# Performance work log

Hardware: AMD Instinct MI355X
Metric: run time of the kernel (lower is better)

Reference implementation:

```python
import jax, jax.numpy as jnp
import numpy as np

NUM_HEADS = 16
D_MODEL = 1024
DEPTH = D_MODEL // NUM_HEADS


def rope_sincos(seq_len, depth):
    # standard RoPE: inv_freq over even dims, sin/cos tiled to full depth
    inv_freq = 1.0 / (10000.0 ** (jnp.arange(0, depth, 2, dtype=jnp.float32) / depth))
    ang = jnp.arange(seq_len, dtype=jnp.float32)[:, None] * inv_freq[None, :]  # [S, depth/2]
    sin = jnp.concatenate([jnp.sin(ang), jnp.sin(ang)], axis=-1)  # [S, depth]
    cos = jnp.concatenate([jnp.cos(ang), jnp.cos(ang)], axis=-1)
    return sin, cos


def apply_rope(x, sin, cos):
    # x: [B,H,S,depth]; rotate-half formulation
    half = x.shape[-1] // 2
    x1, x2 = x[..., :half], x[..., half:]
    rot = jnp.concatenate([-x2, x1], axis=-1)
    return x * cos + rot * sin


def setup_inputs() -> dict:
    key = jax.random.key(0)
    ks = jax.random.split(key, 5)
    s = 1.0 / np.sqrt(D_MODEL)
    return {
        "x": jax.random.normal(ks[0], (2, 2048, D_MODEL), dtype=jnp.float32),
        "wq": jax.random.normal(ks[1], (D_MODEL, D_MODEL), dtype=jnp.float32) * s,
        "bq": jnp.zeros((D_MODEL,), jnp.float32),
        "wk": jax.random.normal(ks[2], (D_MODEL, D_MODEL), dtype=jnp.float32) * s,
        "bk": jnp.zeros((D_MODEL,), jnp.float32),
        "wv": jax.random.normal(ks[3], (D_MODEL, D_MODEL), dtype=jnp.float32) * s,
        "bv": jnp.zeros((D_MODEL,), jnp.float32),
        "wo": jax.random.normal(ks[4], (D_MODEL, D_MODEL), dtype=jnp.float32) * s,
        "bo": jnp.zeros((D_MODEL,), jnp.float32),
    }


def reference(x, wq, bq, wk, bk, wv, bv, wo, bo):
    B, S, _ = x.shape

    def split_heads(t):  # [B,S,D] -> [B,H,S,depth]
        return t.reshape(B, S, NUM_HEADS, DEPTH).transpose(0, 2, 1, 3)

    Q = split_heads(x @ wq + bq)
    K = split_heads(x @ wk + bk)
    V = split_heads(x @ wv + bv)

    sin, cos = rope_sincos(S, DEPTH)  # [S, depth], broadcasts over B,H
    Q = apply_rope(Q, sin, cos)
    K = apply_rope(K, sin, cos)

    scores = jnp.einsum("bhqd,bhkd->bhqk", Q, K) / jnp.sqrt(jnp.float32(DEPTH))
    weights = jax.nn.softmax(scores, axis=-1)
    out = jnp.einsum("bhqk,bhkd->bhqd", weights, V)
    out = out.transpose(0, 2, 1, 3).reshape(B, S, D_MODEL)
    return out @ wo + bo
```

## Files before the change

### kernel.cpp

```cpp
#include <hip/hip_runtime.h>

#define DM 1024
#define SEQ 2048
#define NH 16
#define DH 64
#define BATCH 2

typedef _Float16 half_t;
typedef _Float16 half8 __attribute__((ext_vector_type(8)));
typedef _Float16 half4 __attribute__((ext_vector_type(4)));
typedef __fp16 f16x2 __attribute__((ext_vector_type(2)));
typedef unsigned u32x2 __attribute__((ext_vector_type(2)));
typedef unsigned u32x4 __attribute__((ext_vector_type(4)));
typedef float f32x4 __attribute__((ext_vector_type(4)));

__device__ __forceinline__ f32x4 mfma16(half8 a, half8 b, f32x4 c) {
  return __builtin_amdgcn_mfma_f32_16x16x32_f16(a, b, c, 0, 0, 0);
}
__device__ __forceinline__ f32x4 mfma16k16(half4 a, half4 b, f32x4 c) {
  return __builtin_amdgcn_mfma_f32_16x16x16f16(a, b, c, 0, 0, 0);
}

__device__ __forceinline__ void gl2lds16(const half_t* g, half_t* l) {
  __builtin_amdgcn_global_load_lds((const __attribute__((address_space(1))) void*)g,
                                   (__attribute__((address_space(3))) void*)l, 16, 0, 0);
}


__global__ __launch_bounds__(256)
void prep_kernel(const float* __restrict__ x,
                 const float* __restrict__ w0, const float* __restrict__ w1,
                 const float* __restrict__ w2, const float* __restrict__ w3,
                 half_t* __restrict__ xh,
                 half_t* __restrict__ o0, half_t* __restrict__ o1,
                 half_t* __restrict__ o2, half_t* __restrict__ o3,
                 float* __restrict__ st, float* __restrict__ ct) {
  __shared__ float tile[32][33];
  const int lid = blockIdx.x;
  const int tid = threadIdx.x;
  if (lid < 4096) {
    int i = (lid * 256 + tid) * 4;
    float4 v = *(const float4*)(x + i);
    half4 h = { (half_t)v.x, (half_t)v.y, (half_t)v.z, (half_t)v.w };
    *(half4*)(xh + i) = h;
  } else if (lid < 8192) {
    int l = lid - 4096;
    int z = l >> 10;
    int by = (l >> 5) & 31, bx = l & 31;
    const float* w = (z == 0) ? w0 : (z == 1) ? w1 : (z == 2) ? w2 : w3;
    half_t* o = (z == 0) ? o0 : (z == 1) ? o1 : (z == 2) ? o2 : o3;
    int tx = tid & 31, ty0 = tid >> 5;
    int bxx = bx * 32, byy = by * 32;
#pragma unroll
    for (int i = 0; i < 4; i++) {
      int ty = ty0 + i * 8;
      tile[ty][tx] = w[(size_t)(byy + ty) * DM + bxx + tx];
    }
    __syncthreads();
#pragma unroll
    for (int i = 0; i < 4; i++) {
      int ty = ty0 + i * 8;
      o[(size_t)(bxx + ty) * DM + byy + tx] = (half_t)tile[tx][ty];
    }
  } else {
    int idx = (lid - 8192) * 256 + tid;
    int s = idx >> 5, i = idx & 31;
    float freq = exp2f(-(float)i * (13.287712379549449f / 32.0f));
    float ang = (float)s * freq;
    st[idx] = sinf(ang);
    ct[idx] = cosf(ang);
  }
}


__global__ __launch_bounds__(256)
void qkv_kernel(const half_t* __restrict__ xh,
                const half_t* __restrict__ wtq, const half_t* __restrict__ wtk,
                const half_t* __restrict__ wtv,
                const float* __restrict__ bq, const float* __restrict__ bk,
                const float* __restrict__ bv,
                const float* __restrict__ st, const float* __restrict__ ctab,
                half_t* __restrict__ Qh, half_t* __restrict__ Kh, half_t* __restrict__ Vt) {
  const int tid = threadIdx.x;
  const int wid = tid >> 6, lane = tid & 63;
  const int l16 = lane & 15, quad = lane >> 4;
  const int m0 = blockIdx.y * 128, n0 = blockIdx.x * 128;
  const int g = blockIdx.z;
  const half_t* wt = (g == 0) ? wtq : (g == 1) ? wtk : wtv;
  const float* bias = (g == 0) ? bq : (g == 1) ? bk : bv;
  __shared__ __align__(16) char smem[32768];
  f32x4 acc[4][4] = {};
  const int wrow = (wid >> 1) * 64, wcol = (wid & 1) * 64;

  const int ar0 = tid >> 2,          ab0 = (tid & 3) ^ ((ar0 >> 1) & 3);
  const int ar1 = (tid + 256) >> 2,  ab1 = (tid & 3) ^ ((ar1 >> 1) & 3);
  const int swz = (l16 >> 1) & 3;

  {
    half_t* As = (half_t*)smem;
    half_t* Bs = (half_t*)(smem + 16384);
    gl2lds16(&xh[(size_t)(m0 + ar0) * DM + ab0 * 8], &As[tid * 8]);
    gl2lds16(&xh[(size_t)(m0 + ar1) * DM + ab1 * 8], &As[(tid + 256) * 8]);
    gl2lds16(&wt[(size_t)(n0 + ar0) * DM + ab0 * 8], &Bs[tid * 8]);
    gl2lds16(&wt[(size_t)(n0 + ar1) * DM + ab1 * 8], &Bs[(tid + 256) * 8]);
  }
  __syncthreads();

  int cur = 0;
  for (int k0 = 0; k0 < DM; k0 += 32) {
    if (k0 + 32 < DM) {
      half_t* Asn = (half_t*)(smem + (cur ^ 1) * 8192);
      half_t* Bsn = (half_t*)(smem + 16384 + (cur ^ 1) * 8192);
      const int kn = k0 + 32;
      gl2lds16(&xh[(size_t)(m0 + ar0) * DM + kn + ab0 * 8], &Asn[tid * 8]);
      gl2lds16(&xh[(size_t)(m0 + ar1) * DM + kn + ab1 * 8], &Asn[(tid + 256) * 8]);
      gl2lds16(&wt[(size_t)(n0 + ar0) * DM + kn + ab0 * 8], &Bsn[tid * 8]);
      gl2lds16(&wt[(size_t)(n0 + ar1) * DM + kn + ab1 * 8], &Bsn[(tid + 256) * 8]);
    }
    const half_t* Asc = (const half_t*)(smem + cur * 8192);
    const half_t* Bsc = (const half_t*)(smem + 16384 + cur * 8192);
    half8 a[4], b[4];
#pragma unroll
    for (int rt = 0; rt < 4; rt++)
      a[rt] = *(const half8*)&Asc[((wrow + rt * 16 + l16) * 4 + (quad ^ swz)) * 8];
#pragma unroll
    for (int ct = 0; ct < 4; ct++)
      b[ct] = *(const half8*)&Bsc[((wcol + ct * 16 + l16) * 4 + (quad ^ swz)) * 8];
#pragma unroll
    for (int rt = 0; rt < 4; rt++)
#pragma unroll
      for (int ct = 0; ct < 4; ct++)
        acc[rt][ct] = mfma16(a[rt], b[ct], acc[rt][ct]);
    __syncthreads();
    cur ^= 1;
  }

  const int h = (n0 + wcol) >> 6;
  const float qscale = 0.125f * 1.44269504089f;
  float bv4[4];
#pragma unroll
  for (int ct = 0; ct < 4; ct++) bv4[ct] = bias[n0 + wcol + ct * 16 + l16];

  if (g == 2) {
    half_t* vt = (half_t*)(smem + wid * 8192);
#pragma unroll
    for (int rt = 0; rt < 4; rt++)
#pragma unroll
      for (int ct = 0; ct < 4; ct++) {
        half4 hv;
#pragma unroll
        for (int r = 0; r < 4; r++) hv[r] = (half_t)(acc[rt][ct][r] + bv4[ct]);
        int row = ct * 16 + l16;
        int colu = rt * 2 + (quad >> 1);
        *(half4*)&vt[row * 64 + ((colu ^ (row & 7)) * 8) + (quad & 1) * 4] = hv;
      }
    const int sb = m0 + wrow;
    const int bb = sb >> 11, s0 = sb & 2047;
    half_t* dstv = Vt + (size_t)(bb * NH + h) * DH * SEQ;
#pragma unroll
    for (int i = 0; i < 8; i++) {
      int d = i * 8 + (lane >> 3), c = lane & 7;
      half8 v = *(const half8*)&vt[d * 64 + ((c ^ (d & 7)) * 8)];
      *(half8*)&dstv[(size_t)d * SEQ + s0 + c * 8] = v;
    }
  } else {
    half_t* dst = (g == 0) ? Qh : Kh;
#pragma unroll
    for (int rt = 0; rt < 4; rt++) {
#pragma unroll
      for (int r = 0; r < 4; r++) {
        int m = m0 + wrow + rt * 16 + quad * 4 + r;
        int bb = m >> 11, s = m & 2047;
        float v0 = acc[rt][0][r] + bv4[0];
        float v1 = acc[rt][1][r] + bv4[1];
        float v2 = acc[rt][2][r] + bv4[2];
        float v3 = acc[rt][3][r] + bv4[3];
        float sn0 = st[s * 32 + l16], cs0 = ctab[s * 32 + l16];
        float sn1 = st[s * 32 + 16 + l16], cs1 = ctab[s * 32 + 16 + l16];
        float o0 = v0 * cs0 - v2 * sn0;
        float o1 = v1 * cs1 - v3 * sn1;
        float o2 = v2 * cs0 + v0 * sn0;
        float o3 = v3 * cs1 + v1 * sn1;
        if (g == 0) { o0 *= qscale; o1 *= qscale; o2 *= qscale; o3 *= qscale; }
        size_t base = ((size_t)(bb * NH + h) * SEQ + s) * DH;
        dst[base + l16]      = (half_t)o0;
        dst[base + 16 + l16] = (half_t)o1;
        dst[base + 32 + l16] = (half_t)o2;
        dst[base + 48 + l16] = (half_t)o3;
      }
    }
  }
}


__global__ __launch_bounds__(256)
void attn_kernel(const half_t* __restrict__ Qh, const half_t* __restrict__ Kh,
                 const half_t* __restrict__ Vt, half_t* __restrict__ AO) {
  const int tid = threadIdx.x;
  const int wid = tid >> 6, lane = tid & 63;
  const int l16 = lane & 15, quad = lane >> 4;
  const int lid = blockIdx.x;
  const int bh = lid & 31, qt = lid >> 5;
  const int bb = bh >> 4, h = bh & 15;
  const int q0 = qt * 128 + wid * 32;
  const half_t* Q = Qh + (size_t)bh * SEQ * DH;
  const half_t* K = Kh + (size_t)bh * SEQ * DH;
  const half_t* V = Vt + (size_t)bh * DH * SEQ;
  __shared__ __align__(16) half_t Ks[2][64 * 64];
  __shared__ __align__(16) half_t Vs[2][64 * 64];

  const int r0 = tid >> 3,         c0 = (tid & 7) ^ (r0 & 7);
  const int r1 = (tid + 256) >> 3, c1 = (tid & 7) ^ (r1 & 7);
  const int sw0 = ((quad ^ (l16 & 7)) * 8);
  const int sw1 = (((quad + 4) ^ (l16 & 7)) * 8);

  const half_t* gK0 = &K[(size_t)r0 * DH + c0 * 8];
  const half_t* gK1 = &K[(size_t)r1 * DH + c1 * 8];
  const half_t* gV0 = &V[(size_t)r0 * SEQ + c0 * 8];
  const half_t* gV1 = &V[(size_t)r1 * SEQ + c1 * 8];

  half8 aqA[2], aqB[2];
#pragma unroll
  for (int rt = 0; rt < 2; rt++) {
    aqA[rt] = *(const half8*)&Q[(size_t)(q0 + rt * 16 + l16) * DH + quad * 8];
    aqB[rt] = *(const half8*)&Q[(size_t)(q0 + rt * 16 + l16) * DH + 32 + quad * 8];
  }

  f32x4 o[2][4] = {};
  f32x4 vsum[2] = {};
  const f32x4 cinit = {-12.f, -12.f, -12.f, -12.f};

  gl2lds16(gK0, &Ks[0][tid * 8]);
  gl2lds16(gK1, &Ks[0][(tid + 256) * 8]);
  gl2lds16(gV0, &Vs[0][tid * 8]);
  gl2lds16(gV1, &Vs[0][(tid + 256) * 8]);
  __syncthreads();

  int cur = 0;
  for (int kb0 = 0; kb0 < SEQ; kb0 += 64) {
    const bool pf = (kb0 + 64 < SEQ);
    u32x4 rk0, rk1, rv0, rv1;
    if (pf) {
      const int kb = kb0 + 64;
      rk0 = *(const u32x4*)(gK0 + (size_t)kb * DH);
      rk1 = *(const u32x4*)(gK1 + (size_t)kb * DH);
      rv0 = *(const u32x4*)(gV0 + kb);
      rv1 = *(const u32x4*)(gV1 + kb);
    }
    const half_t* ksrc = Ks[cur];
    const half_t* vsrc = Vs[cur];

    f32x4 z[2][4];
    __builtin_amdgcn_s_setprio(1);
#pragma unroll
    for (int kt = 0; kt < 4; kt++) {
      const half_t* krow = &ksrc[(kt * 16 + l16) * 64];
      half8 b0 = *(const half8*)&krow[sw0];
      half8 b1 = *(const half8*)&krow[sw1];
#pragma unroll
      for (int rt = 0; rt < 2; rt++) {
        f32x4 zz = cinit;
        zz = mfma16(b0, aqA[rt], zz);
        zz = mfma16(b1, aqB[rt], zz);
        z[rt][kt] = zz;
      }
    }
    __builtin_amdgcn_s_setprio(0);

    half4 pa[2][4];
#pragma unroll
    for (int rt = 0; rt < 2; rt++)
#pragma unroll
      for (int kt = 0; kt < 4; kt++) {
        f32x4 p;
#pragma unroll
        for (int r = 0; r < 4; r++) p[r] = __builtin_amdgcn_exp2f(z[rt][kt][r]);
        vsum[rt] += p;
        f16x2 lo = __builtin_amdgcn_cvt_pkrtz(p[0], p[1]);
        f16x2 hi = __builtin_amdgcn_cvt_pkrtz(p[2], p[3]);
        u32x2 w = { __builtin_bit_cast(unsigned, lo), __builtin_bit_cast(unsigned, hi) };
        pa[rt][kt] = __builtin_bit_cast(half4, w);
      }

    __builtin_amdgcn_s_setprio(1);
#pragma unroll
    for (int dt = 0; dt < 4; dt++) {
      const int row = dt * 16 + l16;
      const half_t* vrow = &vsrc[row * 64 + (quad & 1) * 4];
#pragma unroll
      for (int kt = 0; kt < 4; kt++) {
        half4 bv = *(const half4*)&vrow[((kt * 2 + (quad >> 1)) ^ (l16 & 7)) * 8];
#pragma unroll
        for (int rt = 0; rt < 2; rt++)
          o[rt][dt] = mfma16k16(pa[rt][kt], bv, o[rt][dt]);
      }
    }
    __builtin_amdgcn_s_setprio(0);

    if (pf) {
      const int nxt = cur ^ 1;
      *(u32x4*)&Ks[nxt][tid * 8] = rk0;
      *(u32x4*)&Ks[nxt][(tid + 256) * 8] = rk1;
      *(u32x4*)&Vs[nxt][tid * 8] = rv0;
      *(u32x4*)&Vs[nxt][(tid + 256) * 8] = rv1;
    }
    __syncthreads();
    cur ^= 1;
  }

  float linv[2][4];
#pragma unroll
  for (int rt = 0; rt < 2; rt++) {
    float s = (vsum[rt][0] + vsum[rt][1]) + (vsum[rt][2] + vsum[rt][3]);
    s += __shfl_xor(s, 16);
    s += __shfl_xor(s, 32);
#pragma unroll
    for (int r = 0; r < 4; r++) linv[rt][r] = 1.f / __shfl(s, quad * 4 + r);
  }
#pragma unroll
  for (int rt = 0; rt < 2; rt++)
#pragma unroll
    for (int dt = 0; dt < 4; dt++)
#pragma unroll
      for (int r = 0; r < 4; r++) {
        int srow = q0 + rt * 16 + quad * 4 + r;
        AO[((size_t)bb * SEQ + srow) * DM + h * DH + dt * 16 + l16] =
            (half_t)(o[rt][dt][r] * linv[rt][r]);
      }
}


__global__ __launch_bounds__(256)
void out_kernel(const half_t* __restrict__ AO, const half_t* __restrict__ wto,
                const float* __restrict__ bo, float* __restrict__ out) {
  const int tid = threadIdx.x;
  const int wid = tid >> 6, lane = tid & 63;
  const int l16 = lane & 15, quad = lane >> 4;
  const int m0 = blockIdx.y * 128, n0 = blockIdx.x * 64;
  __shared__ __align__(16) char smem[24576];
  f32x4 acc[4][2] = {};
  const int wrow = (wid >> 1) * 64, wcol = (wid & 1) * 32;

  const int ar0 = tid >> 2,         ab0 = (tid & 3) ^ ((ar0 >> 1) & 3);
  const int ar1 = (tid + 256) >> 2, ab1 = (tid & 3) ^ ((ar1 >> 1) & 3);
  const int swz = (l16 >> 1) & 3;

  {
    half_t* As = (half_t*)smem;
    half_t* Bs = (half_t*)(smem + 16384);
    gl2lds16(&AO[(size_t)(m0 + ar0) * DM + ab0 * 8], &As[tid * 8]);
    gl2lds16(&AO[(size_t)(m0 + ar1) * DM + ab1 * 8], &As[(tid + 256) * 8]);
    gl2lds16(&wto[(size_t)(n0 + ar0) * DM + ab0 * 8], &Bs[tid * 8]);
  }
  __syncthreads();

  int cur = 0;
  for (int k0 = 0; k0 < DM; k0 += 32) {
    if (k0 + 32 < DM) {
      half_t* Asn = (half_t*)(smem + (cur ^ 1) * 8192);
      half_t* Bsn = (half_t*)(smem + 16384 + (cur ^ 1) * 4096);
      const int kn = k0 + 32;
      gl2lds16(&AO[(size_t)(m0 + ar0) * DM + kn + ab0 * 8], &Asn[tid * 8]);
      gl2lds16(&AO[(size_t)(m0 + ar1) * DM + kn + ab1 * 8], &Asn[(tid + 256) * 8]);
      gl2lds16(&wto[(size_t)(n0 + ar0) * DM + kn + ab0 * 8], &Bsn[tid * 8]);
    }
    const half_t* Asc = (const half_t*)(smem + cur * 8192);
    const half_t* Bsc = (const half_t*)(smem + 16384 + cur * 4096);
    half8 a[4], b[2];
#pragma unroll
    for (int rt = 0; rt < 4; rt++)
      a[rt] = *(const half8*)&Asc[((wrow + rt * 16 + l16) * 4 + (quad ^ swz)) * 8];
#pragma unroll
    for (int ct = 0; ct < 2; ct++)
      b[ct] = *(const half8*)&Bsc[((wcol + ct * 16 + l16) * 4 + (quad ^ swz)) * 8];
#pragma unroll
    for (int rt = 0; rt < 4; rt++)
#pragma unroll
      for (int ct = 0; ct < 2; ct++)
        acc[rt][ct] = mfma16(a[rt], b[ct], acc[rt][ct]);
    __syncthreads();
    cur ^= 1;
  }
  float bv2[2];
#pragma unroll
  for (int ct = 0; ct < 2; ct++) bv2[ct] = bo[n0 + wcol + ct * 16 + l16];
#pragma unroll
  for (int rt = 0; rt < 4; rt++)
#pragma unroll
    for (int r = 0; r < 4; r++) {
      int m = m0 + wrow + rt * 16 + quad * 4 + r;
#pragma unroll
      for (int ct = 0; ct < 2; ct++)
        out[(size_t)m * DM + n0 + wcol + ct * 16 + l16] = acc[rt][ct][r] + bv2[ct];
    }
}


extern "C" void kernel_launch(void* const* d_in, const int* in_sizes, int n_in,
                              void* d_out, int out_size, void* d_ws, size_t ws_size,
                              hipStream_t stream) {
  (void)in_sizes; (void)n_in; (void)out_size; (void)ws_size;
  const float* x  = (const float*)d_in[0];
  const float* wq = (const float*)d_in[1];
  const float* bq = (const float*)d_in[2];
  const float* wk = (const float*)d_in[3];
  const float* bk = (const float*)d_in[4];
  const float* wv = (const float*)d_in[5];
  const float* bv = (const float*)d_in[6];
  const float* wo = (const float*)d_in[7];
  const float* bo = (const float*)d_in[8];
  char* ws = (char*)d_ws;
  const size_t MB = 1u << 20;
  half_t* xh  = (half_t*)(ws + 0);
  half_t* AO  = (half_t*)(ws + 0);
  half_t* wtq = (half_t*)(ws + 8 * MB);
  half_t* wtk = (half_t*)(ws + 10 * MB);
  half_t* wtv = (half_t*)(ws + 12 * MB);
  half_t* wto = (half_t*)(ws + 14 * MB);
  float*  st  = (float*)(ws + 16 * MB);
  float*  ctb = (float*)(ws + 16 * MB + 256 * 1024);
  half_t* Qh  = (half_t*)(ws + 17 * MB);
  half_t* Kh  = (half_t*)(ws + 25 * MB);
  half_t* Vt  = (half_t*)(ws + 33 * MB);
  float* out = (float*)d_out;

  prep_kernel<<<8448, 256, 0, stream>>>(x, wq, wk, wv, wo, xh, wtq, wtk, wtv, wto, st, ctb);
  qkv_kernel<<<dim3(8, 32, 3), 256, 0, stream>>>(xh, wtq, wtk, wtv, bq, bk, bv, st, ctb, Qh, Kh, Vt);
  attn_kernel<<<512, 256, 0, stream>>>(Qh, Kh, Vt, AO);
  out_kernel<<<dim3(16, 32), 256, 0, stream>>>(AO, wto, bo, out);
}
```

Measured before the change: 194.0 us.

## Use 1024-thread attention blocks with 16 query rows per wave

The attention kernel moves from 256-thread blocks, where each wave owns 32 query rows, to 1024-thread blocks, where each of 16 waves owns 16 rows. Each block now covers 256 queries, so every staged K/V tile is shared by twice as many queries. The K/V load is split so half the threads fetch K and half fetch V, one 16-byte chunk each. The setprio hints are removed, and each wave now has half the MFMA work per LDS read, which lowers per-wave reuse of the loaded K/V fragments. The grid halves to 256 blocks, which may underfill the 256 CUs and makes the per-tile barrier span 16 waves.

New measurement: 195.3 us. About the same (+0.7%).

```diff
diff --git a/kernel.cpp b/kernel.cpp
--- a/kernel.cpp
+++ b/kernel.cpp
@@ -193,7 +193,7 @@
 }
 
 
-__global__ __launch_bounds__(256)
+__global__ __launch_bounds__(1024)
 void attn_kernel(const half_t* __restrict__ Qh, const half_t* __restrict__ Kh,
                  const half_t* __restrict__ Vt, half_t* __restrict__ AO) {
   const int tid = threadIdx.x;
@@ -202,87 +202,68 @@
   const int lid = blockIdx.x;
   const int bh = lid & 31, qt = lid >> 5;
   const int bb = bh >> 4, h = bh & 15;
-  const int q0 = qt * 128 + wid * 32;
+  const int q0 = qt * 256 + wid * 16;
   const half_t* Q = Qh + (size_t)bh * SEQ * DH;
   const half_t* K = Kh + (size_t)bh * SEQ * DH;
   const half_t* V = Vt + (size_t)bh * DH * SEQ;
   __shared__ __align__(16) half_t Ks[2][64 * 64];
   __shared__ __align__(16) half_t Vs[2][64 * 64];
 
-  const int r0 = tid >> 3,         c0 = (tid & 7) ^ (r0 & 7);
-  const int r1 = (tid + 256) >> 3, c1 = (tid & 7) ^ (r1 & 7);
+  const int slot = tid & 511;
+  const int sr = slot >> 3, sc = (slot & 7) ^ (sr & 7);
+  const bool isK = (tid < 512);
+  const half_t* gptr = isK ? &K[(size_t)sr * DH + sc * 8]
+                           : &V[(size_t)sr * SEQ + sc * 8];
+  const int ginc = isK ? 64 * DH : 64;
+  half_t* lbase = (isK ? &Ks[0][0] : &Vs[0][0]) + slot * 8;
+
   const int sw0 = ((quad ^ (l16 & 7)) * 8);
   const int sw1 = (((quad + 4) ^ (l16 & 7)) * 8);
 
-  const half_t* gK0 = &K[(size_t)r0 * DH + c0 * 8];
-  const half_t* gK1 = &K[(size_t)r1 * DH + c1 * 8];
-  const half_t* gV0 = &V[(size_t)r0 * SEQ + c0 * 8];
-  const half_t* gV1 = &V[(size_t)r1 * SEQ + c1 * 8];
-
-  half8 aqA[2], aqB[2];
-#pragma unroll
-  for (int rt = 0; rt < 2; rt++) {
-    aqA[rt] = *(const half8*)&Q[(size_t)(q0 + rt * 16 + l16) * DH + quad * 8];
-    aqB[rt] = *(const half8*)&Q[(size_t)(q0 + rt * 16 + l16) * DH + 32 + quad * 8];
-  }
-
-  f32x4 o[2][4] = {};
-  f32x4 vsum[2] = {};
+  half8 aqA = *(const half8*)&Q[(size_t)(q0 + l16) * DH + quad * 8];
+  half8 aqB = *(const half8*)&Q[(size_t)(q0 + l16) * DH + 32 + quad * 8];
+
+  f32x4 o[4] = {};
+  f32x4 vsum = {};
   const f32x4 cinit = {-12.f, -12.f, -12.f, -12.f};
 
-  gl2lds16(gK0, &Ks[0][tid * 8]);
-  gl2lds16(gK1, &Ks[0][(tid + 256) * 8]);
-  gl2lds16(gV0, &Vs[0][tid * 8]);
-  gl2lds16(gV1, &Vs[0][(tid + 256) * 8]);
+  gl2lds16(gptr, lbase);
+  gptr += ginc;
   __syncthreads();
 
   int cur = 0;
   for (int kb0 = 0; kb0 < SEQ; kb0 += 64) {
     const bool pf = (kb0 + 64 < SEQ);
-    u32x4 rk0, rk1, rv0, rv1;
-    if (pf) {
-      const int kb = kb0 + 64;
-      rk0 = *(const u32x4*)(gK0 + (size_t)kb * DH);
-      rk1 = *(const u32x4*)(gK1 + (size_t)kb * DH);
-      rv0 = *(const u32x4*)(gV0 + kb);
-      rv1 = *(const u32x4*)(gV1 + kb);
-    }
+    u32x4 rg;
+    if (pf) rg = *(const u32x4*)gptr;
     const half_t* ksrc = Ks[cur];
     const half_t* vsrc = Vs[cur];
 
-    f32x4 z[2][4];
-    __builtin_amdgcn_s_setprio(1);
+    f32x4 z[4];
 #pragma unroll
     for (int kt = 0; kt < 4; kt++) {
       const half_t* krow = &ksrc[(kt * 16 + l16) * 64];
       half8 b0 = *(const half8*)&krow[sw0];
       half8 b1 = *(const half8*)&krow[sw1];
-#pragma unroll
-      for (int rt = 0; rt < 2; rt++) {
-        f32x4 zz = cinit;
-        zz = mfma16(b0, aqA[rt], zz);
-        zz = mfma16(b1, aqB[rt], zz);
-        z[rt][kt] = zz;
-      }
-    }
-    __builtin_amdgcn_s_setprio(0);
-
-    half4 pa[2][4];
-#pragma unroll
-    for (int rt = 0; rt < 2; rt++)
-#pragma unroll
-      for (int kt = 0; kt < 4; kt++) {
-        f32x4 p;
-#pragma unroll
-        for (int r = 0; r < 4; r++) p[r] = __builtin_amdgcn_exp2f(z[rt][kt][r]);
-        vsum[rt] += p;
-        f16x2 lo = __builtin_amdgcn_cvt_pkrtz(p[0], p[1]);
-        f16x2 hi = __builtin_amdgcn_cvt_pkrtz(p[2], p[3]);
-        u32x2 w = { __builtin_bit_cast(unsigned, lo), __builtin_bit_cast(unsigned, hi) };
-        pa[rt][kt] = __builtin_bit_cast(half4, w);
-      }
-
-    __builtin_amdgcn_s_setprio(1);
+      f32x4 zz = cinit;
+      zz = mfma16(b0, aqA, zz);
+      zz = mfma16(b1, aqB, zz);
+      z[kt] = zz;
+    }
+
+    half4 pa[4];
+#pragma unroll
+    for (int kt = 0; kt < 4; kt++) {
+      f32x4 p;
+#pragma unroll
+      for (int r = 0; r < 4; r++) p[r] = __builtin_amdgcn_exp2f(z[kt][r]);
+      vsum += p;
+      f16x2 lo = __builtin_amdgcn_cvt_pkrtz(p[0], p[1]);
+      f16x2 hi = __builtin_amdgcn_cvt_pkrtz(p[2], p[3]);
+      u32x2 w = { __builtin_bit_cast(unsigned, lo), __builtin_bit_cast(unsigned, hi) };
+      pa[kt] = __builtin_bit_cast(half4, w);
+    }
+
 #pragma unroll
     for (int dt = 0; dt < 4; dt++) {
       const int row = dt * 16 + l16;
@@ -290,43 +271,34 @@
 #pragma unroll
       for (int kt = 0; kt < 4; kt++) {
         half4 bv = *(const half4*)&vrow[((kt * 2 + (quad >> 1)) ^ (l16 & 7)) * 8];
-#pragma unroll
-        for (int rt = 0; rt < 2; rt++)
-          o[rt][dt] = mfma16k16(pa[rt][kt], bv, o[rt][dt]);
+        o[dt] = mfma16k16(pa[kt], bv, o[dt]);
       }
     }
-    __builtin_amdgcn_s_setprio(0);
 
     if (pf) {
-      const int nxt = cur ^ 1;
-      *(u32x4*)&Ks[nxt][tid * 8] = rk0;
-      *(u32x4*)&Ks[nxt][(tid + 256) * 8] = rk1;
-      *(u32x4*)&Vs[nxt][tid * 8] = rv0;
-      *(u32x4*)&Vs[nxt][(tid + 256) * 8] = rv1;
+      *(u32x4*)(lbase + (cur ^ 1) * 4096) = rg;
+      gptr += ginc;
     }
     __syncthreads();
     cur ^= 1;
   }
 
-  float linv[2][4];
-#pragma unroll
-  for (int rt = 0; rt < 2; rt++) {
-    float s = (vsum[rt][0] + vsum[rt][1]) + (vsum[rt][2] + vsum[rt][3]);
+  float linv[4];
+  {
+    float s = (vsum[0] + vsum[1]) + (vsum[2] + vsum[3]);
     s += __shfl_xor(s, 16);
     s += __shfl_xor(s, 32);
 #pragma unroll
-    for (int r = 0; r < 4; r++) linv[rt][r] = 1.f / __shfl(s, quad * 4 + r);
-  }
-#pragma unroll
-  for (int rt = 0; rt < 2; rt++)
-#pragma unroll
-    for (int dt = 0; dt < 4; dt++)
-#pragma unroll
-      for (int r = 0; r < 4; r++) {
-        int srow = q0 + rt * 16 + quad * 4 + r;
-        AO[((size_t)bb * SEQ + srow) * DM + h * DH + dt * 16 + l16] =
-            (half_t)(o[rt][dt][r] * linv[rt][r]);
-      }
+    for (int r = 0; r < 4; r++) linv[r] = 1.f / __shfl(s, quad * 4 + r);
+  }
+#pragma unroll
+  for (int dt = 0; dt < 4; dt++)
+#pragma unroll
+    for (int r = 0; r < 4; r++) {
+      int srow = q0 + quad * 4 + r;
+      AO[((size_t)bb * SEQ + srow) * DM + h * DH + dt * 16 + l16] =
+          (half_t)(o[dt][r] * linv[r]);
+    }
 }
 
 
@@ -426,6 +398,6 @@
 
   prep_kernel<<<8448, 256, 0, stream>>>(x, wq, wk, wv, wo, xh, wtq, wtk, wtv, wto, st, ctb);
   qkv_kernel<<<dim3(8, 32, 3), 256, 0, stream>>>(xh, wtq, wtk, wtv, bq, bk, bv, st, ctb, Qh, Kh, Vt);
-  attn_kernel<<<512, 256, 0, stream>>>(Qh, Kh, Vt, AO);
+  attn_kernel<<<256, 1024, 0, stream>>>(Qh, Kh, Vt, AO);
   out_kernel<<<dim3(16, 32), 256, 0, stream>>>(AO, wto, bo, out);
 }
```
